# Performance work log

Measured on AMD Instinct MI355X. Metric: run time of the kernel, lower is better.

Reference implementation:

```python
import math
import jax, jax.numpy as jnp
import numpy as np

B, N, E, R = 1024, 200, 256, 256

def _layernorm(x, g, b, eps=1e-5):
    mu = x.mean(-1, keepdims=True)
    var = ((x - mu) ** 2).mean(-1, keepdims=True)
    return (x - mu) / jnp.sqrt(var + eps) * g + b

def setup_inputs() -> dict:
    key = jax.random.key(0)
    ks = jax.random.split(key, 16)
    d = {}
    d["e_emb"] = jax.random.normal(ks[0], (B, E), jnp.float32)
    d["nb_rel"] = jax.random.normal(ks[1], (B, N, R), jnp.float32)
    d["delta_t"] = jax.random.uniform(ks[2], (B, N), jnp.float32) * 10.0
    d["r_emb"] = jax.random.normal(ks[3], (B, R), jnp.float32)
    d["hist_mask"] = jax.random.randint(ks[4], (B, N), 0, 2).astype(bool)
    d["rel_w"] = jax.random.normal(ks[5], (E, R), jnp.float32) / math.sqrt(R)
    d["log_tau1"] = jnp.asarray(1.0, jnp.float32)
    d["log_tau2"] = jnp.asarray(2.5, jnp.float32)
    d["sharpness"] = jnp.asarray(1.5, jnp.float32)
    d["log_gamma"] = jnp.asarray(-2.0, jnp.float32)
    d["attn_w"] = jax.random.normal(ks[6], (3, E, E), jnp.float32) / math.sqrt(E)
    d["sp_w"] = jax.random.normal(ks[7], (3, E, 6 * E), jnp.float32) / math.sqrt(6 * E)
    d["sp_b"] = jnp.zeros((3, E), jnp.float32)
    d["ln_g"] = jnp.ones((3, E), jnp.float32)
    d["ln_b"] = jnp.zeros((3, E), jnp.float32)
    d["csq_w"] = jax.random.normal(ks[8], (E, R), jnp.float32) / math.sqrt(R)
    d["csq_b"] = jnp.zeros((E,), jnp.float32)
    d["csl_w"] = jax.random.normal(ks[9], (3, E), jnp.float32) / math.sqrt(E)
    d["csl_b"] = jnp.zeros((3,), jnp.float32)
    d["on_g"] = jnp.ones((E,), jnp.float32)
    d["on_b"] = jnp.zeros((E,), jnp.float32)
    return d

def _pna_one_scale(msgs, mask, e_emb, q_key, attn_w, sp_w, sp_b, ln_g, ln_b):
    # msgs: [B,N,E], mask: [B,N] bool, e_emb: [B,E], q_key: [B,E]
    valid_f = mask[..., None].astype(msgs.dtype)
    n_valid = jnp.maximum(mask.astype(msgs.dtype).sum(1, keepdims=True), 1.0)  # [B,1]
    msgs_v = msgs * valid_f
    mean_v = msgs_v.sum(1) / n_valid
    max_v = msgs_v.max(1)
    min_v = jnp.clip(jnp.where(mask[..., None], msgs, 10000.0).min(1), -10000.0, 10000.0)
    sq_m = (jnp.clip(msgs_v, -10.0, 10.0) ** 2).sum(1) / n_valid
    std_v = jnp.sqrt(jnp.maximum(sq_m - mean_v ** 2, 1e-6))
    q_proj = q_key @ attn_w.T  # [B,E]
    attn_raw = jnp.einsum('bne,be->bn', msgs, q_proj) / math.sqrt(msgs.shape[-1])
    attn_raw = jnp.where(mask, attn_raw, -10000.0)
    all_invalid = ~mask.any(1, keepdims=True)  # [B,1]
    attn_raw = jnp.where(all_invalid, 0.0, attn_raw)
    attn_p = jax.nn.softmax(attn_raw, axis=-1)
    attn_v = jnp.einsum('bn,bne->be', attn_p, msgs)
    feats = jnp.concatenate([mean_v, max_v, min_v, std_v, attn_v, e_emb], axis=-1)  # [B,6E]
    h = feats @ sp_w.T + sp_b
    h = _layernorm(h, ln_g, ln_b)
    return jax.nn.gelu(h, approximate=False)  # dropout = identity (eval mode)

def reference(e_emb, nb_rel, delta_t, r_emb, hist_mask, rel_w, log_tau1, log_tau2,
              sharpness, log_gamma, attn_w, sp_w, sp_b, ln_g, ln_b,
              csq_w, csq_b, csl_w, csl_b, on_g, on_b):
    msgs = jnp.einsum('bnr,er->bne', nb_rel, rel_w)
    gamma = jnp.exp(log_gamma)
    decay = jnp.exp(-gamma * jnp.maximum(delta_t, 0.0))
    msgs_dec = msgs * decay[..., None]
    tau1 = jnp.exp(log_tau1)
    tau2 = jnp.exp(log_tau2) + tau1
    sharp = jnp.clip(sharpness, 0.1, 5.0)
    w_fine = jax.nn.sigmoid(-sharp * (delta_t - tau1))
    w_coarse = jax.nn.sigmoid(sharp * (delta_t - tau2))
    w_mid = jnp.maximum(1.0 - w_fine - w_coarse, 0.0)
    scale_w = jnp.stack([w_fine, w_mid, w_coarse])  # [3,B,N]
    m_scales = msgs_dec[None] * scale_w[..., None]  # [3,B,N,E]
    q_key = r_emb @ rel_w.T  # [B,E]
    pna_v = jax.vmap(_pna_one_scale, in_axes=(0, None, None, None, 0, 0, 0, 0, 0))
    scales = pna_v(m_scales, hist_mask, e_emb, q_key, attn_w, sp_w, sp_b, ln_g, ln_b)  # [3,B,E]
    sq = r_emb @ csq_w.T + csq_b  # [B,E]
    logits = sq @ csl_w.T + csl_b  # [B,3]
    weights = jax.nn.softmax(logits, axis=-1)
    out = jnp.einsum('bs,sbe->be', weights, scales)
    return _layernorm(out, on_g, on_b)  # drop = identity (eval)
```

## Files before the change

kernel.cpp:

```cpp
#include <hip/hip_runtime.h>
#include <math.h>

#define B_   1024
#define N_   200
#define NR_  208
#define NT_  13
#define E_   256
#define R_   256
#define K6_  1536

typedef __attribute__((ext_vector_type(8))) short bf16x8;
typedef __attribute__((ext_vector_type(4))) float f32x4;

__device__ __forceinline__ unsigned short f2bf(float f) {
  unsigned int u = __float_as_uint(f);
  u += 0x7fffu + ((u >> 16) & 1u);
  return (unsigned short)(u >> 16);
}

__device__ __forceinline__ float gelu_exact(float x) {
  return 0.5f * x * (1.f + erff(x * 0.70710678118654752f));
}

__global__ __launch_bounds__(256) void k_cast(const float* __restrict__ rel_w,
                                              const float* __restrict__ sp_w,
                                              unsigned short* __restrict__ rw_bf,
                                              unsigned short* __restrict__ spw_bf) {
  int idx = blockIdx.x * 256 + threadIdx.x;
  if (idx < E_ * R_) rw_bf[idx] = f2bf(rel_w[idx]);
  int j = idx - E_ * R_;
  if (j >= 0 && j < 3 * E_ * K6_) spw_bf[j] = f2bf(sp_w[j]);
}

__global__ __launch_bounds__(256) void k_prep(
    const float* __restrict__ r_emb, const float* __restrict__ rel_w,
    const float* __restrict__ csq_w, const float* __restrict__ csq_b,
    const float* __restrict__ csl_w, const float* __restrict__ csl_b,
    const float* __restrict__ attn_w,
    float* __restrict__ t_ws, float* __restrict__ wts) {
  __shared__ __align__(16) float re[4][256];
  __shared__ __align__(16) float qk[4][256];
  __shared__ __align__(16) float sqs[4][256];
  __shared__ __align__(16) float qp[3][4][256];
  __shared__ float lg[4][3];
  int b0 = blockIdx.x * 4;
  int tid = threadIdx.x;
  int e = tid;
#pragma unroll
  for (int i = 0; i < 4; ++i)
    re[i][tid] = r_emb[(size_t)(b0 + i) * 256 + tid];
  __syncthreads();
  {
    float qkv[4], sv[4];
#pragma unroll
    for (int i = 0; i < 4; ++i) { qkv[i] = 0.f; sv[i] = 0.f; }
    const float4* w4 = (const float4*)(rel_w) + (size_t)e * 64;
    const float4* c4 = (const float4*)(csq_w) + (size_t)e * 64;
    for (int r = 0; r < 64; ++r) {
      float4 w = w4[r];
      float4 c = c4[r];
#pragma unroll
      for (int i = 0; i < 4; ++i) {
        float4 x = ((const float4*)re[i])[r];
        qkv[i] += w.x * x.x + w.y * x.y + w.z * x.z + w.w * x.w;
        sv[i] += c.x * x.x + c.y * x.y + c.z * x.z + c.w * x.w;
      }
    }
    float cb = csq_b[e];
#pragma unroll
    for (int i = 0; i < 4; ++i) {
      qk[i][e] = qkv[i];
      sqs[i][e] = sv[i] + cb;
    }
  }
  __syncthreads();
  if (tid < 12) {
    int i = tid / 3, k = tid % 3;
    float acc = csl_b[k];
    for (int ee = 0; ee < 256; ++ee) acc += sqs[i][ee] * csl_w[k * 256 + ee];
    lg[i][k] = acc;
  }
  __syncthreads();
  if (tid < 4) {
    float l0 = lg[tid][0], l1 = lg[tid][1], l2 = lg[tid][2];
    float m = fmaxf(l0, fmaxf(l1, l2));
    float e0 = expf(l0 - m), e1 = expf(l1 - m), e2 = expf(l2 - m);
    float inv = 1.f / (e0 + e1 + e2);
    wts[(b0 + tid) * 4 + 0] = e0 * inv;
    wts[(b0 + tid) * 4 + 1] = e1 * inv;
    wts[(b0 + tid) * 4 + 2] = e2 * inv;
  }
  {
    float qpv[3][4];
#pragma unroll
    for (int s = 0; s < 3; ++s)
#pragma unroll
      for (int i = 0; i < 4; ++i) qpv[s][i] = 0.f;
#pragma unroll
    for (int s = 0; s < 3; ++s) {
      const float4* a4 = (const float4*)(attn_w) + ((size_t)s * 256 + e) * 64;
      for (int r = 0; r < 64; ++r) {
        float4 w = a4[r];
#pragma unroll
        for (int i = 0; i < 4; ++i) {
          float4 x = ((const float4*)qk[i])[r];
          qpv[s][i] += w.x * x.x + w.y * x.y + w.z * x.z + w.w * x.w;
        }
      }
    }
    __syncthreads();
#pragma unroll
    for (int s = 0; s < 3; ++s)
#pragma unroll
      for (int i = 0; i < 4; ++i) qp[s][i][e] = qpv[s][i];
  }
  __syncthreads();
  {
    int r = tid;
    float tacc[3][4];
#pragma unroll
    for (int s = 0; s < 3; ++s)
#pragma unroll
      for (int i = 0; i < 4; ++i) tacc[s][i] = 0.f;
    for (int e4 = 0; e4 < 64; ++e4) {
      float4 qv[3][4];
#pragma unroll
      for (int s = 0; s < 3; ++s)
#pragma unroll
        for (int i = 0; i < 4; ++i)
          qv[s][i] = ((const float4*)qp[s][i])[e4];
#pragma unroll
      for (int j = 0; j < 4; ++j) {
        float w = rel_w[(size_t)(e4 * 4 + j) * 256 + r];
#pragma unroll
        for (int s = 0; s < 3; ++s)
#pragma unroll
          for (int i = 0; i < 4; ++i) {
            float q = (j == 0) ? qv[s][i].x : (j == 1) ? qv[s][i].y
                      : (j == 2) ? qv[s][i].z : qv[s][i].w;
            tacc[s][i] = fmaf(q, w, tacc[s][i]);
          }
      }
    }
#pragma unroll
    for (int s = 0; s < 3; ++s)
#pragma unroll
      for (int i = 0; i < 4; ++i)
        t_ws[((size_t)s * B_ + b0 + i) * 256 + r] = tacc[s][i];
  }
}

__global__ __launch_bounds__(1024, 4) void k1_main(
    const float* __restrict__ nb_rel, const float* __restrict__ delta_t,
    const unsigned char* __restrict__ hm_raw, const float* __restrict__ e_emb,
    const float* __restrict__ p_lt1, const float* __restrict__ p_lt2,
    const float* __restrict__ p_sh, const float* __restrict__ p_lgm,
    const unsigned short* __restrict__ rw_bf, const float* __restrict__ t_ws,
    unsigned short* __restrict__ feats) {
  __shared__ __align__(16) struct {
    unsigned int a[NR_ * 132];
    float c[3][NR_];
    float p[3][NR_];
    float nmeta[NR_ * 12];
  } sm;
  int b = blockIdx.x;
  int tid = threadIdx.x;
  int lane = tid & 63, wave = tid >> 6;
  int row16 = lane & 15, quad = lane >> 4;

  int hasNZoff = 0, hasFP = 0;
  {
    unsigned char cc = hm_raw[tid];
    if ((tid & 3) != 0 && cc != 0) {
      hasNZoff = 1;
      if (cc == 0x3Fu || cc == 0x80u) hasFP = 1;
    }
  }
  int cntNZ = __syncthreads_count(hasNZoff);
  int cntFP = __syncthreads_count(hasFP);
  int mmode = (cntNZ == 0) ? 0 : (cntFP > 0 ? 2 : 1);

  float tau1 = __expf(p_lt1[0]);
  float tau2 = __expf(p_lt2[0]) + tau1;
  float sharp = fminf(fmaxf(p_sh[0], 0.1f), 5.0f);
  float gamma = __expf(p_lgm[0]);

  bool mk = false;
  if (tid < NR_) {
    float mf = 0.f, c0 = 0.f, c1 = 0.f, c2 = 0.f;
    if (tid < N_) {
      size_t mi = (size_t)b * N_ + tid;
      if (mmode == 0)      mk = ((const int*)hm_raw)[mi] != 0;
      else if (mmode == 1) mk = hm_raw[mi] != 0;
      else                 mk = ((const float*)hm_raw)[mi] != 0.f;
      float dt = delta_t[mi];
      mf = mk ? 1.f : 0.f;
      float decay = __expf(-gamma * fmaxf(dt, 0.f));
      float wf = 1.f / (1.f + __expf(sharp * (dt - tau1)));
      float wc = 1.f / (1.f + __expf(-sharp * (dt - tau2)));
      float wm = fmaxf(1.f - wf - wc, 0.f);
      c0 = decay * wf; c1 = decay * wm; c2 = decay * wc;
    }
    sm.c[0][tid] = c0; sm.c[1][tid] = c1; sm.c[2][tid] = c2;
    f32x4 w0, w1;
    w0[0] = mf * c0; w0[1] = mf * c1; w0[2] = mf * c2; w0[3] = mk ? 0.f : 1e4f;
    w1[0] = 0.f; w1[1] = 0.f; w1[2] = 0.f; w1[3] = mf;
    *(f32x4*)&sm.nmeta[tid * 12]     = w0;
    *(f32x4*)&sm.nmeta[tid * 12 + 4] = w1;
  }
  int cnt = __syncthreads_count(mk ? 1 : 0);
  float nvf = fmaxf((float)cnt, 1.f);
  bool allinv = (cnt == 0);

  {
    const float* src = nb_rel + (size_t)b * N_ * 256;
    float4 xs[NT_];
#pragma unroll
    for (int i = 0; i < NT_; ++i) {
      int n = i * 16 + wave;
      int gn = (n < N_) ? n : (N_ - 1);
      xs[i] = *(const float4*)(src + (size_t)gn * 256 + lane * 4);
    }
#pragma unroll
    for (int i = 0; i < NT_; ++i) {
      uint2 pk;
      pk.x = (unsigned int)f2bf(xs[i].x) | ((unsigned int)f2bf(xs[i].y) << 16);
      pk.y = (unsigned int)f2bf(xs[i].z) | ((unsigned int)f2bf(xs[i].w) << 16);
      *(uint2*)&sm.a[(i * 16 + wave) * 132 + lane * 2] = pk;
    }
  }
  __syncthreads();

  if (wave < NT_) {
    bf16x8 tfrag[8];
    const float* tp = t_ws + ((size_t)row16 * B_ + b) * 256;
#pragma unroll
    for (int ks = 0; ks < 8; ++ks) {
      bf16x8 tv = {0, 0, 0, 0, 0, 0, 0, 0};
      if (row16 < 3) {
        const float* q = tp + ks * 32 + quad * 8;
#pragma unroll
        for (int j = 0; j < 8; ++j) tv[j] = (short)f2bf(q[j]);
      }
      tfrag[ks] = tv;
    }
    f32x4 acc;
#pragma unroll
    for (int cc = 0; cc < 4; ++cc) acc[cc] = 0.f;
#pragma unroll
    for (int ks = 0; ks < 8; ++ks) {
      bf16x8 af = *(const bf16x8*)&sm.a[(wave * 16 + row16) * 132 + ks * 16 + quad * 4];
      acc = __builtin_amdgcn_mfma_f32_16x16x32_bf16(af, tfrag[ks], acc, 0, 0, 0);
    }
    if (row16 < 3) {
#pragma unroll
      for (int rg = 0; rg < 4; ++rg) {
        int n = wave * 16 + quad * 4 + rg;
        float cw = sm.c[row16][n];
        float mf = sm.nmeta[n * 12 + 7];
        float l = cw * acc[rg] * 0.0625f;
        l = (mf > 0.5f) ? l : -1e4f;
        if (allinv) l = (n < N_) ? 0.f : -1e4f;
        sm.p[row16][n] = l;
      }
    }
  } else if (wave == NT_) {
    for (int i = lane; i < 256; i += 64) {
      unsigned short v = f2bf(e_emb[(size_t)b * 256 + i]);
      feats[((size_t)0 * B_ + b) * K6_ + 1280 + i] = v;
      feats[((size_t)1 * B_ + b) * K6_ + 1280 + i] = v;
      feats[((size_t)2 * B_ + b) * K6_ + 1280 + i] = v;
    }
  }

  bf16x8 bfr[8];
  {
    int e = wave * 16 + row16;
#pragma unroll
    for (int ks = 0; ks < 8; ++ks)
      bfr[ks] = *(const bf16x8*)(rw_bf + (size_t)e * 256 + ks * 32 + quad * 8);
  }
  __syncthreads();

  if (wave < 3) {
    int s = wave;
    float m = -1e30f;
    for (int n = lane; n < NR_; n += 64) m = fmaxf(m, sm.p[s][n]);
#pragma unroll
    for (int o = 32; o >= 1; o >>= 1) m = fmaxf(m, __shfl_xor(m, o, 64));
    float ssum = 0.f;
    for (int n = lane; n < NR_; n += 64) {
      float ev = __expf(sm.p[s][n] - m);
      sm.p[s][n] = ev;
      ssum += ev;
    }
#pragma unroll
    for (int o = 32; o >= 1; o >>= 1) ssum += __shfl_xor(ssum, o, 64);
    float inv = 1.f / ssum;
    for (int n = lane; n < NR_; n += 64)
      sm.nmeta[n * 12 + 4 + s] = sm.p[s][n] * inv * sm.c[s][n];
  }
  __syncthreads();

  float s_mean[3], s_mx[3], s_mn[3], s_sq[3], s_av[3];
#pragma unroll
  for (int s = 0; s < 3; ++s) {
    s_mean[s] = 0.f; s_mx[s] = -1e30f; s_mn[s] = 1e30f;
    s_sq[s] = 0.f; s_av[s] = 0.f;
  }

  for (int nt = 0; nt < NT_; ++nt) {
    f32x4 acc;
#pragma unroll
    for (int cc = 0; cc < 4; ++cc) acc[cc] = 0.f;
#pragma unroll
    for (int ks = 0; ks < 8; ++ks) {
      bf16x8 af = *(const bf16x8*)&sm.a[(nt * 16 + row16) * 132 + ks * 16 + quad * 4];
      acc = __builtin_amdgcn_mfma_f32_16x16x32_bf16(af, bfr[ks], acc, 0, 0, 0);
    }
    int nb = nt * 16 + quad * 4;
#pragma unroll
    for (int rg = 0; rg < 4; ++rg) {
      const float* nm = &sm.nmeta[(size_t)(nb + rg) * 12];
      f32x4 w0 = *(const f32x4*)nm;
      f32x4 w1 = *(const f32x4*)(nm + 4);
      float m = acc[rg];
#pragma unroll
      for (int s = 0; s < 3; ++s) {
        float vm = w0[s] * m;
        s_mean[s] += vm;
        s_mx[s] = fmaxf(s_mx[s], vm);
        s_mn[s] = fminf(s_mn[s], fmaf(w0[s], m, w0[3]));
        float cv = fminf(fmaxf(vm, -10.f), 10.f);
        s_sq[s] = fmaf(cv, cv, s_sq[s]);
        s_av[s] = fmaf(w1[s], m, s_av[s]);
      }
    }
  }

#pragma unroll
  for (int s = 0; s < 3; ++s) {
    float vmean = s_mean[s];
    vmean += __shfl_xor(vmean, 16, 64); vmean += __shfl_xor(vmean, 32, 64);
    float vmx = s_mx[s];
    vmx = fmaxf(vmx, __shfl_xor(vmx, 16, 64)); vmx = fmaxf(vmx, __shfl_xor(vmx, 32, 64));
    float vmn = s_mn[s];
    vmn = fminf(vmn, __shfl_xor(vmn, 16, 64)); vmn = fminf(vmn, __shfl_xor(vmn, 32, 64));
    float vsq = s_sq[s];
    vsq += __shfl_xor(vsq, 16, 64); vsq += __shfl_xor(vsq, 32, 64);
    float vav = s_av[s];
    vav += __shfl_xor(vav, 16, 64); vav += __shfl_xor(vav, 32, 64);
    if (lane < 16) {
      int e = wave * 16 + lane;
      size_t base = ((size_t)s * B_ + b) * K6_;
      float meanv = vmean / nvf;
      float stdv = sqrtf(fmaxf(vsq / nvf - meanv * meanv, 1e-6f));
      float mnv = fminf(fmaxf(vmn, -1e4f), 1e4f);
      feats[base + e] = f2bf(meanv);
      feats[base + 256 + e] = f2bf(vmx);
      feats[base + 512 + e] = f2bf(mnv);
      feats[base + 768 + e] = f2bf(stdv);
      feats[base + 1024 + e] = f2bf(vav);
    }
  }
}

__global__ __launch_bounds__(256) void k2_kernel(
    const unsigned short* __restrict__ feats, const unsigned short* __restrict__ spw_bf,
    const float* __restrict__ sp_b, float* __restrict__ hbuf) {
  __shared__ __align__(16) unsigned int a[16 * 132];
  int id = blockIdx.x;
  int s = id >> 7;
  int rem = id & 127;
  int b0 = (rem >> 1) * 16;
  int e0 = (rem & 1) * 128;
  int tid = threadIdx.x, lane = tid & 63, wave = tid >> 6;
  int row16 = lane & 15, quad = lane >> 4;
  f32x4 acc[2];
#pragma unroll
  for (int t = 0; t < 2; ++t)
#pragma unroll
    for (int cc = 0; cc < 4; ++cc) acc[t][cc] = 0.f;

  for (int kc = 0; kc < 6; ++kc) {
    __syncthreads();
    for (int j = tid; j < 512; j += 256) {
      int rw = j >> 5, ck = j & 31;
      bf16x8 v = *(const bf16x8*)(feats + ((size_t)s * B_ + b0 + rw) * K6_ + kc * 256 + ck * 8);
      *(bf16x8*)((unsigned short*)&a[rw * 132] + ck * 8) = v;
    }
    __syncthreads();
#pragma unroll
    for (int ks = 0; ks < 8; ++ks) {
      bf16x8 af = *(const bf16x8*)&a[row16 * 132 + ks * 16 + quad * 4];
#pragma unroll
      for (int t = 0; t < 2; ++t) {
        int e = e0 + wave * 32 + t * 16 + row16;
        bf16x8 bfr = *(const bf16x8*)(spw_bf + ((size_t)s * E_ + e) * K6_ + kc * 256 + ks * 32 + quad * 8);
        acc[t] = __builtin_amdgcn_mfma_f32_16x16x32_bf16(af, bfr, acc[t], 0, 0, 0);
      }
    }
  }
#pragma unroll
  for (int t = 0; t < 2; ++t) {
    int e = e0 + wave * 32 + t * 16 + row16;
    float bias = sp_b[s * 256 + e];
#pragma unroll
    for (int rg = 0; rg < 4; ++rg) {
      int rw = quad * 4 + rg;
      hbuf[((size_t)s * B_ + b0 + rw) * 256 + e] = acc[t][rg] + bias;
    }
  }
}

__global__ __launch_bounds__(256) void k3_kernel(
    const float* __restrict__ hbuf, const float* __restrict__ wts,
    const float* __restrict__ ln_g, const float* __restrict__ ln_b,
    const float* __restrict__ on_g, const float* __restrict__ on_b,
    float* __restrict__ out) {
  __shared__ float rs[4], rq[4];
  int b = blockIdx.x, tid = threadIdx.x, lane = tid & 63, wave = tid >> 6;
  float o = 0.f;
#pragma unroll
  for (int s = 0; s < 3; ++s) {
    float h = hbuf[((size_t)s * B_ + b) * 256 + tid];
    float sum = h, sq = h * h;
#pragma unroll
    for (int off = 32; off >= 1; off >>= 1) {
      sum += __shfl_xor(sum, off, 64);
      sq += __shfl_xor(sq, off, 64);
    }
    if (lane == 0) { rs[wave] = sum; rq[wave] = sq; }
    __syncthreads();
    float ts = rs[0] + rs[1] + rs[2] + rs[3];
    float tq = rq[0] + rq[1] + rq[2] + rq[3];
    __syncthreads();
    float mu = ts * (1.f / 256.f);
    float var = tq * (1.f / 256.f) - mu * mu;
    float rstd = rsqrtf(var + 1e-5f);
    float v = (h - mu) * rstd * ln_g[s * 256 + tid] + ln_b[s * 256 + tid];
    o += wts[b * 4 + s] * gelu_exact(v);
  }
  float sum = o, sq = o * o;
#pragma unroll
  for (int off = 32; off >= 1; off >>= 1) {
    sum += __shfl_xor(sum, off, 64);
    sq += __shfl_xor(sq, off, 64);
  }
  if (lane == 0) { rs[wave] = sum; rq[wave] = sq; }
  __syncthreads();
  float ts = rs[0] + rs[1] + rs[2] + rs[3];
  float tq = rq[0] + rq[1] + rq[2] + rq[3];
  float mu = ts * (1.f / 256.f);
  float var = tq * (1.f / 256.f) - mu * mu;
  float rstd = rsqrtf(var + 1e-5f);
  out[(size_t)b * 256 + tid] = (o - mu) * rstd * on_g[tid] + on_b[tid];
}

extern "C" void kernel_launch(void* const* d_in, const int* in_sizes, int n_in,
                              void* d_out, int out_size, void* d_ws, size_t ws_size,
                              hipStream_t stream) {
  const float* e_emb   = (const float*)d_in[0];
  const float* nb_rel  = (const float*)d_in[1];
  const float* delta_t = (const float*)d_in[2];
  const float* r_emb   = (const float*)d_in[3];
  const unsigned char* hist_mask = (const unsigned char*)d_in[4];
  const float* rel_w   = (const float*)d_in[5];
  const float* lt1     = (const float*)d_in[6];
  const float* lt2     = (const float*)d_in[7];
  const float* shp     = (const float*)d_in[8];
  const float* lgm     = (const float*)d_in[9];
  const float* attn_w  = (const float*)d_in[10];
  const float* sp_w    = (const float*)d_in[11];
  const float* sp_b    = (const float*)d_in[12];
  const float* ln_g    = (const float*)d_in[13];
  const float* ln_b    = (const float*)d_in[14];
  const float* csq_w   = (const float*)d_in[15];
  const float* csq_b   = (const float*)d_in[16];
  const float* csl_w   = (const float*)d_in[17];
  const float* csl_b   = (const float*)d_in[18];
  const float* on_g    = (const float*)d_in[19];
  const float* on_b    = (const float*)d_in[20];
  float* out = (float*)d_out;

  char* ws = (char*)d_ws;
  unsigned short* rw_bf  = (unsigned short*)(ws + 0);
  unsigned short* spw_bf = (unsigned short*)(ws + 131072);
  float* t_ws   = (float*)(ws + 2490368);
  float* wts    = (float*)(ws + 5636096);
  unsigned short* feats = (unsigned short*)(ws + 5652480);
  float* hbuf   = (float*)(ws + 15089664);

  hipLaunchKernelGGL(k_cast, dim3(4864), dim3(256), 0, stream, rel_w, sp_w, rw_bf, spw_bf);
  hipLaunchKernelGGL(k_prep, dim3(256), dim3(256), 0, stream, r_emb, rel_w, csq_w, csq_b,
                     csl_w, csl_b, attn_w, t_ws, wts);
  hipLaunchKernelGGL(k1_main, dim3(1024), dim3(1024), 0, stream, nb_rel, delta_t, hist_mask,
                     e_emb, lt1, lt2, shp, lgm, rw_bf, t_ws, feats);
  hipLaunchKernelGGL(k2_kernel, dim3(384), dim3(256), 0, stream, feats, spw_bf, sp_b, hbuf);
  hipLaunchKernelGGL(k3_kernel, dim3(1024), dim3(256), 0, stream, hbuf, wts, ln_g, ln_b,
                     on_g, on_b, out);
}
```

Before: 524.9 us.

## Halve k1 shared-memory tile and stream nb_rel in two passes for occupancy

The main kernel now stages only 7 of the 13 neighbor tiles in LDS at a time. It processes the tiles in phases: first-half attention logits, second-half logits, second-half aggregation GEMM, then a reload of the first half for the final GEMMs. This shrinks LDS and register use so launch bounds can request 8 waves per EU instead of 4. The attention query vectors are also precomputed in bf16 with a per-batch layout, and the conversions use packed bf16 intrinsics. The cost is reading nb_rel from global memory twice for the first half and adding extra block barriers.

```diff
diff --git a/kernel.cpp b/kernel.cpp
--- a/kernel.cpp
+++ b/kernel.cpp
@@ -1,4 +1,5 @@
 #include <hip/hip_runtime.h>
+#include <hip/hip_bf16.h>
 #include <math.h>
 
 #define B_   1024
@@ -16,6 +17,14 @@
   unsigned int u = __float_as_uint(f);
   u += 0x7fffu + ((u >> 16) & 1u);
   return (unsigned short)(u >> 16);
+}
+
+__device__ __forceinline__ unsigned int pk_bf(float lo, float hi) {
+  float2 t; t.x = lo; t.y = hi;
+  __hip_bfloat162 h = __float22bfloat162_rn(t);
+  unsigned int u;
+  __builtin_memcpy(&u, &h, 4);
+  return u;
 }
 
 __device__ __forceinline__ float gelu_exact(float x) {
@@ -37,7 +46,7 @@
     const float* __restrict__ csq_w, const float* __restrict__ csq_b,
     const float* __restrict__ csl_w, const float* __restrict__ csl_b,
     const float* __restrict__ attn_w,
-    float* __restrict__ t_ws, float* __restrict__ wts) {
+    unsigned short* __restrict__ t_bf, float* __restrict__ wts) {
   __shared__ __align__(16) float re[4][256];
   __shared__ __align__(16) float qk[4][256];
   __shared__ __align__(16) float sqs[4][256];
@@ -146,19 +155,19 @@
     for (int s = 0; s < 3; ++s)
 #pragma unroll
       for (int i = 0; i < 4; ++i)
-        t_ws[((size_t)s * B_ + b0 + i) * 256 + r] = tacc[s][i];
-  }
-}
-
-__global__ __launch_bounds__(1024, 4) void k1_main(
+        t_bf[((size_t)(b0 + i) * 3 + s) * 256 + r] = f2bf(tacc[s][i]);
+  }
+}
+
+__global__ __launch_bounds__(1024, 8) void k1_main(
     const float* __restrict__ nb_rel, const float* __restrict__ delta_t,
     const unsigned char* __restrict__ hm_raw, const float* __restrict__ e_emb,
     const float* __restrict__ p_lt1, const float* __restrict__ p_lt2,
     const float* __restrict__ p_sh, const float* __restrict__ p_lgm,
-    const unsigned short* __restrict__ rw_bf, const float* __restrict__ t_ws,
+    const unsigned short* __restrict__ rw_bf, const unsigned short* __restrict__ t_bf,
     unsigned short* __restrict__ feats) {
   __shared__ __align__(16) struct {
-    unsigned int a[NR_ * 132];
+    unsigned int a[7 * 16 * 132];
     float c[3][NR_];
     float p[3][NR_];
     float nmeta[NR_ * 12];
@@ -212,37 +221,35 @@
   float nvf = fmaxf((float)cnt, 1.f);
   bool allinv = (cnt == 0);
 
-  {
-    const float* src = nb_rel + (size_t)b * N_ * 256;
-    float4 xs[NT_];
-#pragma unroll
-    for (int i = 0; i < NT_; ++i) {
-      int n = i * 16 + wave;
-      int gn = (n < N_) ? n : (N_ - 1);
-      xs[i] = *(const float4*)(src + (size_t)gn * 256 + lane * 4);
-    }
-#pragma unroll
-    for (int i = 0; i < NT_; ++i) {
+  const float* srcw = nb_rel + (size_t)b * N_ * 256 + lane * 4;
+
+  {
+    float4 xa = *(const float4*)(srcw + (size_t)(wave) * 256);
+    float4 xb = *(const float4*)(srcw + (size_t)(16 + wave) * 256);
+#pragma unroll
+    for (int j = 0; j < 7; ++j) {
       uint2 pk;
-      pk.x = (unsigned int)f2bf(xs[i].x) | ((unsigned int)f2bf(xs[i].y) << 16);
-      pk.y = (unsigned int)f2bf(xs[i].z) | ((unsigned int)f2bf(xs[i].w) << 16);
-      *(uint2*)&sm.a[(i * 16 + wave) * 132 + lane * 2] = pk;
-    }
-  }
-  __syncthreads();
-
-  if (wave < NT_) {
+      pk.x = pk_bf(xa.x, xa.y);
+      pk.y = pk_bf(xa.z, xa.w);
+      *(uint2*)&sm.a[(j * 16 + wave) * 132 + lane * 2] = pk;
+      xa = xb;
+      if (j + 2 < 7)
+        xb = *(const float4*)(srcw + (size_t)((j + 2) * 16 + wave) * 256);
+    }
+  }
+  __syncthreads();
+
+  if (wave < 7) {
     bf16x8 tfrag[8];
-    const float* tp = t_ws + ((size_t)row16 * B_ + b) * 256;
-#pragma unroll
-    for (int ks = 0; ks < 8; ++ks) {
-      bf16x8 tv = {0, 0, 0, 0, 0, 0, 0, 0};
-      if (row16 < 3) {
-        const float* q = tp + ks * 32 + quad * 8;
-#pragma unroll
-        for (int j = 0; j < 8; ++j) tv[j] = (short)f2bf(q[j]);
-      }
-      tfrag[ks] = tv;
+    {
+      int sr = (row16 < 3) ? row16 : 0;
+      const unsigned short* tb = t_bf + ((size_t)b * 3 + sr) * 256 + quad * 8;
+      bf16x8 zer = {0, 0, 0, 0, 0, 0, 0, 0};
+#pragma unroll
+      for (int ks = 0; ks < 8; ++ks) {
+        bf16x8 tv = *(const bf16x8*)(tb + ks * 32);
+        tfrag[ks] = (row16 < 3) ? tv : zer;
+      }
     }
     f32x4 acc;
 #pragma unroll
@@ -264,12 +271,67 @@
         sm.p[row16][n] = l;
       }
     }
-  } else if (wave == NT_) {
+  } else if (wave == 13) {
     for (int i = lane; i < 256; i += 64) {
       unsigned short v = f2bf(e_emb[(size_t)b * 256 + i]);
       feats[((size_t)0 * B_ + b) * K6_ + 1280 + i] = v;
       feats[((size_t)1 * B_ + b) * K6_ + 1280 + i] = v;
       feats[((size_t)2 * B_ + b) * K6_ + 1280 + i] = v;
+    }
+  }
+  __syncthreads();
+
+  {
+    float4 xa = *(const float4*)(srcw + (size_t)(112 + wave) * 256);
+    float4 xb = *(const float4*)(srcw + (size_t)(128 + wave) * 256);
+#pragma unroll
+    for (int j = 0; j < 6; ++j) {
+      uint2 pk;
+      pk.x = pk_bf(xa.x, xa.y);
+      pk.y = pk_bf(xa.z, xa.w);
+      *(uint2*)&sm.a[(j * 16 + wave) * 132 + lane * 2] = pk;
+      xa = xb;
+      if (j + 2 < 6) {
+        int n = 112 + (j + 2) * 16 + wave;
+        int gn = (n < N_) ? n : (N_ - 1);
+        xb = *(const float4*)(srcw + (size_t)gn * 256);
+      }
+    }
+  }
+  __syncthreads();
+
+  if (wave >= 7 && wave < 13) {
+    bf16x8 tfrag[8];
+    {
+      int sr = (row16 < 3) ? row16 : 0;
+      const unsigned short* tb = t_bf + ((size_t)b * 3 + sr) * 256 + quad * 8;
+      bf16x8 zer = {0, 0, 0, 0, 0, 0, 0, 0};
+#pragma unroll
+      for (int ks = 0; ks < 8; ++ks) {
+        bf16x8 tv = *(const bf16x8*)(tb + ks * 32);
+        tfrag[ks] = (row16 < 3) ? tv : zer;
+      }
+    }
+    f32x4 acc;
+#pragma unroll
+    for (int cc = 0; cc < 4; ++cc) acc[cc] = 0.f;
+    int slot = wave - 7;
+#pragma unroll
+    for (int ks = 0; ks < 8; ++ks) {
+      bf16x8 af = *(const bf16x8*)&sm.a[(slot * 16 + row16) * 132 + ks * 16 + quad * 4];
+      acc = __builtin_amdgcn_mfma_f32_16x16x32_bf16(af, tfrag[ks], acc, 0, 0, 0);
+    }
+    if (row16 < 3) {
+#pragma unroll
+      for (int rg = 0; rg < 4; ++rg) {
+        int n = wave * 16 + quad * 4 + rg;
+        float cw = sm.c[row16][n];
+        float mf = sm.nmeta[n * 12 + 7];
+        float l = cw * acc[rg] * 0.0625f;
+        l = (mf > 0.5f) ? l : -1e4f;
+        if (allinv) l = (n < N_) ? 0.f : -1e4f;
+        sm.p[row16][n] = l;
+      }
     }
   }
 
@@ -309,34 +371,52 @@
     s_sq[s] = 0.f; s_av[s] = 0.f;
   }
 
-  for (int nt = 0; nt < NT_; ++nt) {
-    f32x4 acc;
-#pragma unroll
-    for (int cc = 0; cc < 4; ++cc) acc[cc] = 0.f;
-#pragma unroll
-    for (int ks = 0; ks < 8; ++ks) {
-      bf16x8 af = *(const bf16x8*)&sm.a[(nt * 16 + row16) * 132 + ks * 16 + quad * 4];
-      acc = __builtin_amdgcn_mfma_f32_16x16x32_bf16(af, bfr[ks], acc, 0, 0, 0);
-    }
-    int nb = nt * 16 + quad * 4;
-#pragma unroll
-    for (int rg = 0; rg < 4; ++rg) {
-      const float* nm = &sm.nmeta[(size_t)(nb + rg) * 12];
-      f32x4 w0 = *(const f32x4*)nm;
-      f32x4 w1 = *(const f32x4*)(nm + 4);
-      float m = acc[rg];
-#pragma unroll
-      for (int s = 0; s < 3; ++s) {
-        float vm = w0[s] * m;
-        s_mean[s] += vm;
-        s_mx[s] = fmaxf(s_mx[s], vm);
-        s_mn[s] = fminf(s_mn[s], fmaf(w0[s], m, w0[3]));
-        float cv = fminf(fmaxf(vm, -10.f), 10.f);
-        s_sq[s] = fmaf(cv, cv, s_sq[s]);
-        s_av[s] = fmaf(w1[s], m, s_av[s]);
-      }
-    }
-  }
+#define GEMM_TILE(SLOT, NTR) do {                                              \
+    f32x4 acc;                                                                 \
+    acc[0] = 0.f; acc[1] = 0.f; acc[2] = 0.f; acc[3] = 0.f;                    \
+    _Pragma("unroll")                                                          \
+    for (int ks = 0; ks < 8; ++ks) {                                           \
+      bf16x8 af = *(const bf16x8*)&sm.a[((SLOT) * 16 + row16) * 132 + ks * 16 + quad * 4]; \
+      acc = __builtin_amdgcn_mfma_f32_16x16x32_bf16(af, bfr[ks], acc, 0, 0, 0);\
+    }                                                                          \
+    int nb = (NTR) * 16 + quad * 4;                                            \
+    _Pragma("unroll")                                                          \
+    for (int rg = 0; rg < 4; ++rg) {                                           \
+      const float* nm = &sm.nmeta[(size_t)(nb + rg) * 12];                     \
+      f32x4 w0 = *(const f32x4*)nm;                                            \
+      f32x4 w1 = *(const f32x4*)(nm + 4);                                      \
+      float m = acc[rg];                                                       \
+      _Pragma("unroll")                                                        \
+      for (int s = 0; s < 3; ++s) {                                            \
+        float vm = w0[s] * m;                                                  \
+        s_mean[s] += vm;                                                       \
+        s_mx[s] = fmaxf(s_mx[s], vm);                                          \
+        s_mn[s] = fminf(s_mn[s], fmaf(w0[s], m, w0[3]));                       \
+        float cv = fminf(fmaxf(vm, -10.f), 10.f);                              \
+        s_sq[s] = fmaf(cv, cv, s_sq[s]);                                       \
+        s_av[s] = fmaf(w1[s], m, s_av[s]);                                     \
+      }                                                                        \
+    }                                                                          \
+  } while (0)
+
+  {
+    float4 xa = *(const float4*)(srcw + (size_t)(wave) * 256);
+    for (int j = 0; j < 6; ++j) {
+      GEMM_TILE(j, 7 + j);
+      __syncthreads();
+      uint2 pk;
+      pk.x = pk_bf(xa.x, xa.y);
+      pk.y = pk_bf(xa.z, xa.w);
+      *(uint2*)&sm.a[(j * 16 + wave) * 132 + lane * 2] = pk;
+      if (j < 5)
+        xa = *(const float4*)(srcw + (size_t)((j + 1) * 16 + wave) * 256);
+    }
+  }
+  __syncthreads();
+  for (int j = 0; j < 7; ++j) {
+    GEMM_TILE(j, j);
+  }
+#undef GEMM_TILE
 
 #pragma unroll
   for (int s = 0; s < 3; ++s) {
@@ -486,16 +566,16 @@
   char* ws = (char*)d_ws;
   unsigned short* rw_bf  = (unsigned short*)(ws + 0);
   unsigned short* spw_bf = (unsigned short*)(ws + 131072);
-  float* t_ws   = (float*)(ws + 2490368);
-  float* wts    = (float*)(ws + 5636096);
-  unsigned short* feats = (unsigned short*)(ws + 5652480);
-  float* hbuf   = (float*)(ws + 15089664);
+  unsigned short* t_bf   = (unsigned short*)(ws + 2490368);
+  float* wts    = (float*)(ws + 4063232);
+  unsigned short* feats = (unsigned short*)(ws + 4079616);
+  float* hbuf   = (float*)(ws + 13516800);
 
   hipLaunchKernelGGL(k_cast, dim3(4864), dim3(256), 0, stream, rel_w, sp_w, rw_bf, spw_bf);
   hipLaunchKernelGGL(k_prep, dim3(256), dim3(256), 0, stream, r_emb, rel_w, csq_w, csq_b,
-                     csl_w, csl_b, attn_w, t_ws, wts);
+                     csl_w, csl_b, attn_w, t_bf, wts);
   hipLaunchKernelGGL(k1_main, dim3(1024), dim3(1024), 0, stream, nb_rel, delta_t, hist_mask,
-                     e_emb, lt1, lt2, shp, lgm, rw_bf, t_ws, feats);
+                     e_emb, lt1, lt2, shp, lgm, rw_bf, t_bf, feats);
   hipLaunchKernelGGL(k2_kernel, dim3(384), dim3(256), 0, stream, feats, spw_bf, sp_b, hbuf);
   hipLaunchKernelGGL(k3_kernel, dim3(1024), dim3(256), 0, stream, hbuf, wts, ln_g, ln_b,
                      on_g, on_b, out);
```

After: 646.4 us. 23.1% more time.

## Stream nb_rel through double-buffered LDS tiles in two passes instead of full staging

Applied to the files above, without the earlier changes.

k1_main no longer stages all 208 nb_rel rows in LDS. It streams 16-row tiles through a double-buffered LDS ring with a register prefetch of the next tile, and it does this twice: once for the attention-logit MFMA and once for the message statistics. As a result nb_rel is read from global memory twice, and each of the 13 tiles now costs a block barrier. The attention query t_ws is also precomputed as bf16 in [b][s][r] layout, which removes the per-thread conversion. The aim is to shrink LDS use so more blocks fit per CU and to overlap loads with MFMA work, at the price of extra traffic and synchronisation.

```diff
diff --git a/kernel.cpp b/kernel.cpp
--- a/kernel.cpp
+++ b/kernel.cpp
@@ -1,4 +1,5 @@
 #include <hip/hip_runtime.h>
+#include <hip/hip_bf16.h>
 #include <math.h>
 
 #define B_   1024
@@ -16,6 +17,14 @@
   unsigned int u = __float_as_uint(f);
   u += 0x7fffu + ((u >> 16) & 1u);
   return (unsigned short)(u >> 16);
+}
+
+__device__ __forceinline__ unsigned int pk_bf(float lo, float hi) {
+  float2 t; t.x = lo; t.y = hi;
+  __hip_bfloat162 h = __float22bfloat162_rn(t);
+  unsigned int u;
+  __builtin_memcpy(&u, &h, 4);
+  return u;
 }
 
 __device__ __forceinline__ float gelu_exact(float x) {
@@ -37,7 +46,7 @@
     const float* __restrict__ csq_w, const float* __restrict__ csq_b,
     const float* __restrict__ csl_w, const float* __restrict__ csl_b,
     const float* __restrict__ attn_w,
-    float* __restrict__ t_ws, float* __restrict__ wts) {
+    unsigned short* __restrict__ t_bf, float* __restrict__ wts) {
   __shared__ __align__(16) float re[4][256];
   __shared__ __align__(16) float qk[4][256];
   __shared__ __align__(16) float sqs[4][256];
@@ -146,7 +155,7 @@
     for (int s = 0; s < 3; ++s)
 #pragma unroll
       for (int i = 0; i < 4; ++i)
-        t_ws[((size_t)s * B_ + b0 + i) * 256 + r] = tacc[s][i];
+        t_bf[((size_t)(b0 + i) * 3 + s) * 256 + r] = f2bf(tacc[s][i]);
   }
 }
 
@@ -155,10 +164,10 @@
     const unsigned char* __restrict__ hm_raw, const float* __restrict__ e_emb,
     const float* __restrict__ p_lt1, const float* __restrict__ p_lt2,
     const float* __restrict__ p_sh, const float* __restrict__ p_lgm,
-    const unsigned short* __restrict__ rw_bf, const float* __restrict__ t_ws,
+    const unsigned short* __restrict__ rw_bf, const unsigned short* __restrict__ t_bf,
     unsigned short* __restrict__ feats) {
   __shared__ __align__(16) struct {
-    unsigned int a[NR_ * 132];
+    unsigned int a[2 * 16 * 132];
     float c[3][NR_];
     float p[3][NR_];
     float nmeta[NR_ * 12];
@@ -212,59 +221,21 @@
   float nvf = fmaxf((float)cnt, 1.f);
   bool allinv = (cnt == 0);
 
-  {
-    const float* src = nb_rel + (size_t)b * N_ * 256;
-    float4 xs[NT_];
-#pragma unroll
-    for (int i = 0; i < NT_; ++i) {
-      int n = i * 16 + wave;
-      int gn = (n < N_) ? n : (N_ - 1);
-      xs[i] = *(const float4*)(src + (size_t)gn * 256 + lane * 4);
-    }
-#pragma unroll
-    for (int i = 0; i < NT_; ++i) {
-      uint2 pk;
-      pk.x = (unsigned int)f2bf(xs[i].x) | ((unsigned int)f2bf(xs[i].y) << 16);
-      pk.y = (unsigned int)f2bf(xs[i].z) | ((unsigned int)f2bf(xs[i].w) << 16);
-      *(uint2*)&sm.a[(i * 16 + wave) * 132 + lane * 2] = pk;
-    }
-  }
-  __syncthreads();
-
-  if (wave < NT_) {
-    bf16x8 tfrag[8];
-    const float* tp = t_ws + ((size_t)row16 * B_ + b) * 256;
+  const float* srcw = nb_rel + (size_t)b * N_ * 256 + lane * 4;
+
+  bf16x8 tfrag[8];
+  {
+    int sr = (row16 < 3) ? row16 : 0;
+    const unsigned short* tb = t_bf + ((size_t)b * 3 + sr) * 256 + quad * 8;
+    bf16x8 zer = {0, 0, 0, 0, 0, 0, 0, 0};
 #pragma unroll
     for (int ks = 0; ks < 8; ++ks) {
-      bf16x8 tv = {0, 0, 0, 0, 0, 0, 0, 0};
-      if (row16 < 3) {
-        const float* q = tp + ks * 32 + quad * 8;
-#pragma unroll
-        for (int j = 0; j < 8; ++j) tv[j] = (short)f2bf(q[j]);
-      }
-      tfrag[ks] = tv;
-    }
-    f32x4 acc;
-#pragma unroll
-    for (int cc = 0; cc < 4; ++cc) acc[cc] = 0.f;
-#pragma unroll
-    for (int ks = 0; ks < 8; ++ks) {
-      bf16x8 af = *(const bf16x8*)&sm.a[(wave * 16 + row16) * 132 + ks * 16 + quad * 4];
-      acc = __builtin_amdgcn_mfma_f32_16x16x32_bf16(af, tfrag[ks], acc, 0, 0, 0);
-    }
-    if (row16 < 3) {
-#pragma unroll
-      for (int rg = 0; rg < 4; ++rg) {
-        int n = wave * 16 + quad * 4 + rg;
-        float cw = sm.c[row16][n];
-        float mf = sm.nmeta[n * 12 + 7];
-        float l = cw * acc[rg] * 0.0625f;
-        l = (mf > 0.5f) ? l : -1e4f;
-        if (allinv) l = (n < N_) ? 0.f : -1e4f;
-        sm.p[row16][n] = l;
-      }
-    }
-  } else if (wave == NT_) {
+      bf16x8 tv = *(const bf16x8*)(tb + ks * 32);
+      tfrag[ks] = (row16 < 3) ? tv : zer;
+    }
+  }
+
+  if (wave == 15) {
     for (int i = lane; i < 256; i += 64) {
       unsigned short v = f2bf(e_emb[(size_t)b * 256 + i]);
       feats[((size_t)0 * B_ + b) * K6_ + 1280 + i] = v;
@@ -273,6 +244,53 @@
     }
   }
 
+  {
+    float4 x = *(const float4*)(srcw + (size_t)wave * 256);
+    uint2 pk;
+    pk.x = pk_bf(x.x, x.y);
+    pk.y = pk_bf(x.z, x.w);
+    *(uint2*)&sm.a[wave * 132 + lane * 2] = pk;
+  }
+  __syncthreads();
+
+  for (int t = 0; t < NT_; ++t) {
+    float4 xn;
+    if (t < NT_ - 1) {
+      int n = (t + 1) * 16 + wave;
+      int gn = (n < N_) ? n : (N_ - 1);
+      xn = *(const float4*)(srcw + (size_t)gn * 256);
+    }
+    if (wave == t) {
+      f32x4 acc;
+      acc[0] = 0.f; acc[1] = 0.f; acc[2] = 0.f; acc[3] = 0.f;
+      const unsigned int* sa = &sm.a[(t & 1) * 2112];
+#pragma unroll
+      for (int ks = 0; ks < 8; ++ks) {
+        bf16x8 af = *(const bf16x8*)&sa[row16 * 132 + ks * 16 + quad * 4];
+        acc = __builtin_amdgcn_mfma_f32_16x16x32_bf16(af, tfrag[ks], acc, 0, 0, 0);
+      }
+      if (row16 < 3) {
+#pragma unroll
+        for (int rg = 0; rg < 4; ++rg) {
+          int n = t * 16 + quad * 4 + rg;
+          float cw = sm.c[row16][n];
+          float mf = sm.nmeta[n * 12 + 7];
+          float l = cw * acc[rg] * 0.0625f;
+          l = (mf > 0.5f) ? l : -1e4f;
+          if (allinv) l = (n < N_) ? 0.f : -1e4f;
+          sm.p[row16][n] = l;
+        }
+      }
+    }
+    if (t < NT_ - 1) {
+      uint2 pk;
+      pk.x = pk_bf(xn.x, xn.y);
+      pk.y = pk_bf(xn.z, xn.w);
+      *(uint2*)&sm.a[((t + 1) & 1) * 2112 + wave * 132 + lane * 2] = pk;
+    }
+    __syncthreads();
+  }
+
   bf16x8 bfr[8];
   {
     int e = wave * 16 + row16;
@@ -280,8 +298,13 @@
     for (int ks = 0; ks < 8; ++ks)
       bfr[ks] = *(const bf16x8*)(rw_bf + (size_t)e * 256 + ks * 32 + quad * 8);
   }
-  __syncthreads();
-
+  {
+    float4 x = *(const float4*)(srcw + (size_t)wave * 256);
+    uint2 pk;
+    pk.x = pk_bf(x.x, x.y);
+    pk.y = pk_bf(x.z, x.w);
+    *(uint2*)&sm.a[wave * 132 + lane * 2] = pk;
+  }
   if (wave < 3) {
     int s = wave;
     float m = -1e30f;
@@ -309,16 +332,22 @@
     s_sq[s] = 0.f; s_av[s] = 0.f;
   }
 
-  for (int nt = 0; nt < NT_; ++nt) {
+  for (int t = 0; t < NT_; ++t) {
+    float4 xn;
+    if (t < NT_ - 1) {
+      int n = (t + 1) * 16 + wave;
+      int gn = (n < N_) ? n : (N_ - 1);
+      xn = *(const float4*)(srcw + (size_t)gn * 256);
+    }
     f32x4 acc;
-#pragma unroll
-    for (int cc = 0; cc < 4; ++cc) acc[cc] = 0.f;
+    acc[0] = 0.f; acc[1] = 0.f; acc[2] = 0.f; acc[3] = 0.f;
+    const unsigned int* sa = &sm.a[(t & 1) * 2112];
 #pragma unroll
     for (int ks = 0; ks < 8; ++ks) {
-      bf16x8 af = *(const bf16x8*)&sm.a[(nt * 16 + row16) * 132 + ks * 16 + quad * 4];
+      bf16x8 af = *(const bf16x8*)&sa[row16 * 132 + ks * 16 + quad * 4];
       acc = __builtin_amdgcn_mfma_f32_16x16x32_bf16(af, bfr[ks], acc, 0, 0, 0);
     }
-    int nb = nt * 16 + quad * 4;
+    int nb = t * 16 + quad * 4;
 #pragma unroll
     for (int rg = 0; rg < 4; ++rg) {
       const float* nm = &sm.nmeta[(size_t)(nb + rg) * 12];
@@ -336,6 +365,13 @@
         s_av[s] = fmaf(w1[s], m, s_av[s]);
       }
     }
+    if (t < NT_ - 1) {
+      uint2 pk;
+      pk.x = pk_bf(xn.x, xn.y);
+      pk.y = pk_bf(xn.z, xn.w);
+      *(uint2*)&sm.a[((t + 1) & 1) * 2112 + wave * 132 + lane * 2] = pk;
+    }
+    __syncthreads();
   }
 
 #pragma unroll
@@ -486,16 +522,16 @@
   char* ws = (char*)d_ws;
   unsigned short* rw_bf  = (unsigned short*)(ws + 0);
   unsigned short* spw_bf = (unsigned short*)(ws + 131072);
-  float* t_ws   = (float*)(ws + 2490368);
-  float* wts    = (float*)(ws + 5636096);
-  unsigned short* feats = (unsigned short*)(ws + 5652480);
-  float* hbuf   = (float*)(ws + 15089664);
+  unsigned short* t_bf   = (unsigned short*)(ws + 2490368);
+  float* wts    = (float*)(ws + 4063232);
+  unsigned short* feats = (unsigned short*)(ws + 4079616);
+  float* hbuf   = (float*)(ws + 13516800);
 
   hipLaunchKernelGGL(k_cast, dim3(4864), dim3(256), 0, stream, rel_w, sp_w, rw_bf, spw_bf);
   hipLaunchKernelGGL(k_prep, dim3(256), dim3(256), 0, stream, r_emb, rel_w, csq_w, csq_b,
-                     csl_w, csl_b, attn_w, t_ws, wts);
+                     csl_w, csl_b, attn_w, t_bf, wts);
   hipLaunchKernelGGL(k1_main, dim3(1024), dim3(1024), 0, stream, nb_rel, delta_t, hist_mask,
-                     e_emb, lt1, lt2, shp, lgm, rw_bf, t_ws, feats);
+                     e_emb, lt1, lt2, shp, lgm, rw_bf, t_bf, feats);
   hipLaunchKernelGGL(k2_kernel, dim3(384), dim3(256), 0, stream, feats, spw_bf, sp_b, hbuf);
   hipLaunchKernelGGL(k3_kernel, dim3(1024), dim3(256), 0, stream, hbuf, wts, ln_g, ln_b,
                      on_g, on_b, out);
```

Result: slower. 542.7 us (+3.4%).

## Pre-swizzle weights into MFMA fragment layouts and restructure prep and projection kernels

Applied to the files above, without the earlier changes.

The cast kernel now writes rel_w and sp_w in bf16 already arranged in MFMA fragment order, and writes fp32 transposes of rel_w, csq_w and attn_w. This lets the prep kernel read weights coalesced across threads instead of one row per thread. The prep kernel stores the t vectors directly as bf16 in a per-batch layout, so k1 loads them as vector reads without converting. k2 now stages the whole 16x1536 feature tile in LDS once, uses a finer 64-column split (double the blocks) and reads contiguous swizzled weight fragments. The cost is a larger cast kernel and extra workspace for the transposed copies.

```diff
diff --git a/kernel.cpp b/kernel.cpp
--- a/kernel.cpp
+++ b/kernel.cpp
@@ -1,4 +1,5 @@
 #include <hip/hip_runtime.h>
+#include <hip/hip_bf16.h>
 #include <math.h>
 
 #define B_   1024
@@ -18,26 +19,55 @@
   return (unsigned short)(u >> 16);
 }
 
+__device__ __forceinline__ unsigned int pk_bf(float lo, float hi) {
+  float2 t; t.x = lo; t.y = hi;
+  __hip_bfloat162 h = __float22bfloat162_rn(t);
+  unsigned int u;
+  __builtin_memcpy(&u, &h, 4);
+  return u;
+}
+
 __device__ __forceinline__ float gelu_exact(float x) {
   return 0.5f * x * (1.f + erff(x * 0.70710678118654752f));
 }
 
-__global__ __launch_bounds__(256) void k_cast(const float* __restrict__ rel_w,
-                                              const float* __restrict__ sp_w,
-                                              unsigned short* __restrict__ rw_bf,
-                                              unsigned short* __restrict__ spw_bf) {
-  int idx = blockIdx.x * 256 + threadIdx.x;
-  if (idx < E_ * R_) rw_bf[idx] = f2bf(rel_w[idx]);
-  int j = idx - E_ * R_;
-  if (j >= 0 && j < 3 * E_ * K6_) spw_bf[j] = f2bf(sp_w[j]);
+__global__ __launch_bounds__(256) void k_cast(
+    const float* __restrict__ rel_w, const float* __restrict__ sp_w,
+    const float* __restrict__ csq_w, const float* __restrict__ attn_w,
+    unsigned short* __restrict__ rwf, unsigned short* __restrict__ spwf,
+    float* __restrict__ rwT, float* __restrict__ cwT, float* __restrict__ awT) {
+  int o = blockIdx.x * 256 + threadIdx.x;
+  if (o < 65536) {
+    int j = o & 7, r16 = (o >> 3) & 15, quad = (o >> 7) & 3, ks = (o >> 9) & 7, et = o >> 12;
+    rwf[o] = f2bf(rel_w[(size_t)(et * 16 + r16) * 256 + ks * 32 + quad * 8 + j]);
+    return;
+  }
+  o -= 65536;
+  if (o < 1179648) {
+    int j = o & 7, r16 = (o >> 3) & 15, quad = (o >> 7) & 3, ks = (o >> 9) & 7;
+    int rest = o >> 12;
+    int kc = rest % 6, se = rest / 6;
+    int et = se & 15, s = se >> 4;
+    spwf[o] = f2bf(sp_w[(size_t)(s * 256 + et * 16 + r16) * 1536 + kc * 256 + ks * 32 + quad * 8 + j]);
+    return;
+  }
+  o -= 1179648;
+  if (o < 65536) { int r = o >> 8, e = o & 255; rwT[o] = rel_w[(size_t)e * 256 + r]; return; }
+  o -= 65536;
+  if (o < 65536) { int r = o >> 8, e = o & 255; cwT[o] = csq_w[(size_t)e * 256 + r]; return; }
+  o -= 65536;
+  if (o < 196608) {
+    int s = o >> 16, rem = o & 65535, ep = rem >> 8, e = rem & 255;
+    awT[o] = attn_w[((size_t)s * 256 + e) * 256 + ep];
+  }
 }
 
 __global__ __launch_bounds__(256) void k_prep(
-    const float* __restrict__ r_emb, const float* __restrict__ rel_w,
-    const float* __restrict__ csq_w, const float* __restrict__ csq_b,
-    const float* __restrict__ csl_w, const float* __restrict__ csl_b,
-    const float* __restrict__ attn_w,
-    float* __restrict__ t_ws, float* __restrict__ wts) {
+    const float* __restrict__ r_emb, const float* __restrict__ rwT,
+    const float* __restrict__ cwT, const float* __restrict__ awT,
+    const float* __restrict__ csq_b, const float* __restrict__ csl_w,
+    const float* __restrict__ csl_b, const float* __restrict__ rel_w,
+    unsigned short* __restrict__ t_bf, float* __restrict__ wts) {
   __shared__ __align__(16) float re[4][256];
   __shared__ __align__(16) float qk[4][256];
   __shared__ __align__(16) float sqs[4][256];
@@ -54,16 +84,21 @@
     float qkv[4], sv[4];
 #pragma unroll
     for (int i = 0; i < 4; ++i) { qkv[i] = 0.f; sv[i] = 0.f; }
-    const float4* w4 = (const float4*)(rel_w) + (size_t)e * 64;
-    const float4* c4 = (const float4*)(csq_w) + (size_t)e * 64;
-    for (int r = 0; r < 64; ++r) {
-      float4 w = w4[r];
-      float4 c = c4[r];
-#pragma unroll
-      for (int i = 0; i < 4; ++i) {
-        float4 x = ((const float4*)re[i])[r];
-        qkv[i] += w.x * x.x + w.y * x.y + w.z * x.z + w.w * x.w;
-        sv[i] += c.x * x.x + c.y * x.y + c.z * x.z + c.w * x.w;
+    for (int g = 0; g < 64; ++g) {
+      float4 xi[4];
+#pragma unroll
+      for (int i = 0; i < 4; ++i) xi[i] = ((const float4*)re[i])[g];
+#pragma unroll
+      for (int k = 0; k < 4; ++k) {
+        int r = g * 4 + k;
+        float w = rwT[(size_t)r * 256 + e];
+        float c = cwT[(size_t)r * 256 + e];
+#pragma unroll
+        for (int i = 0; i < 4; ++i) {
+          float x = (k == 0) ? xi[i].x : (k == 1) ? xi[i].y : (k == 2) ? xi[i].z : xi[i].w;
+          qkv[i] = fmaf(w, x, qkv[i]);
+          sv[i]  = fmaf(c, x, sv[i]);
+        }
       }
     }
     float cb = csq_b[e];
@@ -96,15 +131,21 @@
     for (int s = 0; s < 3; ++s)
 #pragma unroll
       for (int i = 0; i < 4; ++i) qpv[s][i] = 0.f;
-#pragma unroll
-    for (int s = 0; s < 3; ++s) {
-      const float4* a4 = (const float4*)(attn_w) + ((size_t)s * 256 + e) * 64;
-      for (int r = 0; r < 64; ++r) {
-        float4 w = a4[r];
-#pragma unroll
-        for (int i = 0; i < 4; ++i) {
-          float4 x = ((const float4*)qk[i])[r];
-          qpv[s][i] += w.x * x.x + w.y * x.y + w.z * x.z + w.w * x.w;
+    for (int g = 0; g < 64; ++g) {
+      float4 qf[4];
+#pragma unroll
+      for (int i = 0; i < 4; ++i) qf[i] = ((const float4*)qk[i])[g];
+#pragma unroll
+      for (int k = 0; k < 4; ++k) {
+        int ep = g * 4 + k;
+#pragma unroll
+        for (int s = 0; s < 3; ++s) {
+          float w = awT[((size_t)s * 256 + ep) * 256 + e];
+#pragma unroll
+          for (int i = 0; i < 4; ++i) {
+            float x = (k == 0) ? qf[i].x : (k == 1) ? qf[i].y : (k == 2) ? qf[i].z : qf[i].w;
+            qpv[s][i] = fmaf(w, x, qpv[s][i]);
+          }
         }
       }
     }
@@ -146,7 +187,7 @@
     for (int s = 0; s < 3; ++s)
 #pragma unroll
       for (int i = 0; i < 4; ++i)
-        t_ws[((size_t)s * B_ + b0 + i) * 256 + r] = tacc[s][i];
+        t_bf[((size_t)(b0 + i) * 3 + s) * 256 + r] = f2bf(tacc[s][i]);
   }
 }
 
@@ -155,7 +196,7 @@
     const unsigned char* __restrict__ hm_raw, const float* __restrict__ e_emb,
     const float* __restrict__ p_lt1, const float* __restrict__ p_lt2,
     const float* __restrict__ p_sh, const float* __restrict__ p_lgm,
-    const unsigned short* __restrict__ rw_bf, const float* __restrict__ t_ws,
+    const unsigned short* __restrict__ rwf, const unsigned short* __restrict__ t_bf,
     unsigned short* __restrict__ feats) {
   __shared__ __align__(16) struct {
     unsigned int a[NR_ * 132];
@@ -224,8 +265,8 @@
 #pragma unroll
     for (int i = 0; i < NT_; ++i) {
       uint2 pk;
-      pk.x = (unsigned int)f2bf(xs[i].x) | ((unsigned int)f2bf(xs[i].y) << 16);
-      pk.y = (unsigned int)f2bf(xs[i].z) | ((unsigned int)f2bf(xs[i].w) << 16);
+      pk.x = pk_bf(xs[i].x, xs[i].y);
+      pk.y = pk_bf(xs[i].z, xs[i].w);
       *(uint2*)&sm.a[(i * 16 + wave) * 132 + lane * 2] = pk;
     }
   }
@@ -233,16 +274,15 @@
 
   if (wave < NT_) {
     bf16x8 tfrag[8];
-    const float* tp = t_ws + ((size_t)row16 * B_ + b) * 256;
-#pragma unroll
-    for (int ks = 0; ks < 8; ++ks) {
-      bf16x8 tv = {0, 0, 0, 0, 0, 0, 0, 0};
-      if (row16 < 3) {
-        const float* q = tp + ks * 32 + quad * 8;
-#pragma unroll
-        for (int j = 0; j < 8; ++j) tv[j] = (short)f2bf(q[j]);
+    {
+      int sr = (row16 < 3) ? row16 : 0;
+      const unsigned short* tb = t_bf + ((size_t)b * 3 + sr) * 256 + quad * 8;
+      bf16x8 zer = {0, 0, 0, 0, 0, 0, 0, 0};
+#pragma unroll
+      for (int ks = 0; ks < 8; ++ks) {
+        bf16x8 tv = *(const bf16x8*)(tb + ks * 32);
+        tfrag[ks] = (row16 < 3) ? tv : zer;
       }
-      tfrag[ks] = tv;
     }
     f32x4 acc;
 #pragma unroll
@@ -275,10 +315,9 @@
 
   bf16x8 bfr[8];
   {
-    int e = wave * 16 + row16;
 #pragma unroll
     for (int ks = 0; ks < 8; ++ks)
-      bfr[ks] = *(const bf16x8*)(rw_bf + (size_t)e * 256 + ks * 32 + quad * 8);
+      bfr[ks] = *(const bf16x8*)(rwf + ((((size_t)wave * 8 + ks) * 4 + quad) * 16 + row16) * 8);
   }
   __syncthreads();
 
@@ -366,49 +405,53 @@
 }
 
 __global__ __launch_bounds__(256) void k2_kernel(
-    const unsigned short* __restrict__ feats, const unsigned short* __restrict__ spw_bf,
+    const unsigned short* __restrict__ feats, const unsigned short* __restrict__ spwf,
     const float* __restrict__ sp_b, float* __restrict__ hbuf) {
-  __shared__ __align__(16) unsigned int a[16 * 132];
+  __shared__ __align__(16) unsigned short A[16][1544];
   int id = blockIdx.x;
-  int s = id >> 7;
-  int rem = id & 127;
-  int b0 = (rem >> 1) * 16;
-  int e0 = (rem & 1) * 128;
+  int s = id >> 8;
+  int rem = id & 255;
+  int b0 = (rem >> 2) * 16;
+  int e0 = (rem & 3) * 64;
   int tid = threadIdx.x, lane = tid & 63, wave = tid >> 6;
   int row16 = lane & 15, quad = lane >> 4;
-  f32x4 acc[2];
-#pragma unroll
-  for (int t = 0; t < 2; ++t)
-#pragma unroll
-    for (int cc = 0; cc < 4; ++cc) acc[t][cc] = 0.f;
-
+
+  bf16x8 v[12];
+#pragma unroll
+  for (int t = 0; t < 12; ++t) {
+    int j = tid + t * 256;
+    int rw = j / 192, ck = j % 192;
+    v[t] = *(const bf16x8*)(feats + ((size_t)s * B_ + b0 + rw) * K6_ + ck * 8);
+  }
+#pragma unroll
+  for (int t = 0; t < 12; ++t) {
+    int j = tid + t * 256;
+    int rw = j / 192, ck = j % 192;
+    *(bf16x8*)&A[rw][ck * 8] = v[t];
+  }
+  __syncthreads();
+
+  int et = (e0 >> 4) + wave;
+  const unsigned short* bp = spwf + (((size_t)s * 16 + et) * 6) * 4096;
+  f32x4 acc;
+#pragma unroll
+  for (int cc = 0; cc < 4; ++cc) acc[cc] = 0.f;
+#pragma unroll
   for (int kc = 0; kc < 6; ++kc) {
-    __syncthreads();
-    for (int j = tid; j < 512; j += 256) {
-      int rw = j >> 5, ck = j & 31;
-      bf16x8 v = *(const bf16x8*)(feats + ((size_t)s * B_ + b0 + rw) * K6_ + kc * 256 + ck * 8);
-      *(bf16x8*)((unsigned short*)&a[rw * 132] + ck * 8) = v;
-    }
-    __syncthreads();
 #pragma unroll
     for (int ks = 0; ks < 8; ++ks) {
-      bf16x8 af = *(const bf16x8*)&a[row16 * 132 + ks * 16 + quad * 4];
-#pragma unroll
-      for (int t = 0; t < 2; ++t) {
-        int e = e0 + wave * 32 + t * 16 + row16;
-        bf16x8 bfr = *(const bf16x8*)(spw_bf + ((size_t)s * E_ + e) * K6_ + kc * 256 + ks * 32 + quad * 8);
-        acc[t] = __builtin_amdgcn_mfma_f32_16x16x32_bf16(af, bfr, acc[t], 0, 0, 0);
-      }
-    }
-  }
-#pragma unroll
-  for (int t = 0; t < 2; ++t) {
-    int e = e0 + wave * 32 + t * 16 + row16;
+      bf16x8 af = *(const bf16x8*)&A[row16][kc * 256 + ks * 32 + quad * 8];
+      bf16x8 bf = *(const bf16x8*)(bp + ((size_t)(kc * 8 + ks) * 4 + quad) * 128 + row16 * 8);
+      acc = __builtin_amdgcn_mfma_f32_16x16x32_bf16(af, bf, acc, 0, 0, 0);
+    }
+  }
+  {
+    int e = e0 + wave * 16 + row16;
     float bias = sp_b[s * 256 + e];
 #pragma unroll
     for (int rg = 0; rg < 4; ++rg) {
       int rw = quad * 4 + rg;
-      hbuf[((size_t)s * B_ + b0 + rw) * 256 + e] = acc[t][rg] + bias;
+      hbuf[((size_t)s * B_ + b0 + rw) * 256 + e] = acc[rg] + bias;
     }
   }
 }
@@ -484,19 +527,23 @@
   float* out = (float*)d_out;
 
   char* ws = (char*)d_ws;
-  unsigned short* rw_bf  = (unsigned short*)(ws + 0);
-  unsigned short* spw_bf = (unsigned short*)(ws + 131072);
-  float* t_ws   = (float*)(ws + 2490368);
-  float* wts    = (float*)(ws + 5636096);
-  unsigned short* feats = (unsigned short*)(ws + 5652480);
-  float* hbuf   = (float*)(ws + 15089664);
-
-  hipLaunchKernelGGL(k_cast, dim3(4864), dim3(256), 0, stream, rel_w, sp_w, rw_bf, spw_bf);
-  hipLaunchKernelGGL(k_prep, dim3(256), dim3(256), 0, stream, r_emb, rel_w, csq_w, csq_b,
-                     csl_w, csl_b, attn_w, t_ws, wts);
+  unsigned short* rwf   = (unsigned short*)(ws + 0);
+  unsigned short* spwf  = (unsigned short*)(ws + 131072);
+  unsigned short* t_bf  = (unsigned short*)(ws + 2490368);
+  float* wts    = (float*)(ws + 4063232);
+  unsigned short* feats = (unsigned short*)(ws + 4079616);
+  float* hbuf   = (float*)(ws + 13516800);
+  float* rwT    = (float*)(ws + 16662528);
+  float* cwT    = (float*)(ws + 16924672);
+  float* awT    = (float*)(ws + 17186816);
+
+  hipLaunchKernelGGL(k_cast, dim3(6144), dim3(256), 0, stream, rel_w, sp_w, csq_w, attn_w,
+                     rwf, spwf, rwT, cwT, awT);
+  hipLaunchKernelGGL(k_prep, dim3(256), dim3(256), 0, stream, r_emb, rwT, cwT, awT,
+                     csq_b, csl_w, csl_b, rel_w, t_bf, wts);
   hipLaunchKernelGGL(k1_main, dim3(1024), dim3(1024), 0, stream, nb_rel, delta_t, hist_mask,
-                     e_emb, lt1, lt2, shp, lgm, rw_bf, t_ws, feats);
-  hipLaunchKernelGGL(k2_kernel, dim3(384), dim3(256), 0, stream, feats, spw_bf, sp_b, hbuf);
+                     e_emb, lt1, lt2, shp, lgm, rwf, t_bf, feats);
+  hipLaunchKernelGGL(k2_kernel, dim3(768), dim3(256), 0, stream, feats, spwf, sp_b, hbuf);
   hipLaunchKernelGGL(k3_kernel, dim3(1024), dim3(256), 0, stream, hbuf, wts, ln_g, ln_b,
                      on_g, on_b, out);
 }
```

New measurement: 484.2 us. 7.7% less time.
